# Performance work log

Measured on AMD Instinct MI355X. Metric: run time of the kernel, lower is better.

The kernel has to match this reference:

```python
import jax, jax.numpy as jnp
import numpy as np

B, Tr, P = 256, 512, 128
H, P_STD, P_STATIC, HEAD_H = 128, 32, 16, 64


def _uniform(key, shape, fan_in):
    bound = 1.0 / np.sqrt(fan_in)
    return jax.random.uniform(key, shape, jnp.float32, -bound, bound)


def setup_inputs() -> dict:
    key = jax.random.key(0)
    ks = jax.random.split(key, 16)
    X_raw = jax.random.normal(ks[0], (B, Tr, P), jnp.float32)
    M_raw = (jax.random.uniform(ks[1], (B, Tr, P)) < 0.7).astype(jnp.float32)
    DT_raw = jax.random.uniform(ks[2], (B, Tr, P), jnp.float32)
    STD_agg = jax.random.normal(ks[3], (B, 64, P_STD), jnp.float32)
    Z = jax.random.normal(ks[4], (B, P_STATIC), jnp.float32)
    idx_map = jax.random.randint(ks[5], (B, 64), -1, Tr)  # -1 marks invalid slots
    x_mean = jnp.zeros((P,), jnp.float32)  # non-trainable buffer-like param
    Wd = _uniform(ks[6], (H, P), P)
    bd = _uniform(ks[7], (H,), P)
    Wih = _uniform(ks[8], (3 * H, 2 * P), H)
    bih = _uniform(ks[9], (3 * H,), H)
    Whh = _uniform(ks[10], (3 * H, H), H)
    bhh = _uniform(ks[11], (3 * H,), H)
    W1 = _uniform(ks[12], (HEAD_H, H + P_STD + P_STATIC), H + P_STD + P_STATIC)
    b1 = _uniform(ks[13], (HEAD_H,), H + P_STD + P_STATIC)
    W2 = _uniform(ks[14], (1, HEAD_H), HEAD_H)
    return {"X_raw": X_raw, "M_raw": M_raw, "DT_raw": DT_raw, "STD_agg": STD_agg,
            "Z": Z, "idx_map": idx_map, "x_mean": x_mean, "Wd": Wd, "bd": bd,
            "Wih": Wih, "bih": bih, "Whh": Whh, "bhh": bhh,
            "W1": W1, "b1": b1, "W2": W2}


def reference(X_raw, M_raw, DT_raw, STD_agg, Z, idx_map, x_mean,
              Wd, bd, Wih, bih, Whh, bhh, W1, b1, W2):
    b, tr, p = X_raw.shape
    hdim = Whh.shape[1]

    def step(h, xs):
        x, m, dt = xs  # each [B, p]
        delta = jnp.exp(-jax.nn.softplus(dt))
        x_hat = m * x + (1 - m) * x_mean
        x_dec = m * x + (1 - m) * (delta * x_hat + (1 - delta) * x_mean)
        h_til = jnp.tanh(x_hat @ Wd.T + bd)
        h = delta * h + (1 - delta) * h_til  # requires p == hdim (as in source)
        inp = jnp.concatenate([x_dec, m], axis=-1)  # [B, 2p]
        gi = inp @ Wih.T + bih
        gh = h @ Whh.T + bhh
        gi_r, gi_z, gi_n = jnp.split(gi, 3, axis=-1)
        gh_r, gh_z, gh_n = jnp.split(gh, 3, axis=-1)
        r = jax.nn.sigmoid(gi_r + gh_r)
        z = jax.nn.sigmoid(gi_z + gh_z)
        n = jnp.tanh(gi_n + r * gh_n)
        h = (1 - z) * n + z * h
        return h, h

    h0 = jnp.zeros((b, hdim), X_raw.dtype)
    xs = (jnp.swapaxes(X_raw, 0, 1), jnp.swapaxes(M_raw, 0, 1), jnp.swapaxes(DT_raw, 0, 1))
    _, Hs = jax.lax.scan(step, h0, xs)  # [Tr, B, H]
    H_raw = jnp.swapaxes(Hs, 0, 1)  # [B, Tr, H]

    mask_sel = idx_map >= 0
    idx_safe = jnp.clip(idx_map, 0, None)
    H_agg = jnp.take_along_axis(H_raw, idx_safe[:, :, None], axis=1)
    H_agg = H_agg * mask_sel[:, :, None].astype(H_raw.dtype)  # [B, Ta, H]

    Ta = idx_map.shape[1]
    Zrep = jnp.broadcast_to(Z[:, None, :], (b, Ta, Z.shape[-1]))
    feats = jnp.concatenate([H_agg, STD_agg, Zrep], axis=-1)
    eta = (jax.nn.relu(feats @ W1.T + b1) @ W2.T)[..., 0]  # dropout is identity in eval
    return eta, H_raw, H_agg, mask_sel.astype(X_raw.dtype)
```

## Files before the change

kernel.cpp:

```cpp
#include <hip/hip_runtime.h>
#include <hip/hip_bf16.h>
#include <hip/hip_fp16.h>

#define B_    256
#define TR    512
#define P_    128
#define H_    128
#define NG    384
#define KI    256
#define TA    64
#define PSTD  32
#define PSTAT 16
#define HH    64
#define FDIM  176

#define TB    16
#define NT    (TR/TB)
#define TILE_BYTES 24576

typedef __attribute__((ext_vector_type(8))) short short8;
typedef __attribute__((ext_vector_type(4))) float f32x4;

__device__ __forceinline__ float bf2f(ushort u) {
    union { uint i; float f; } v; v.i = ((uint)u) << 16; return v.f;
}
__device__ __forceinline__ ushort f2bf(float f) {
    union { float f; uint u; } v; v.f = f;
    uint u = v.u;
    uint r = (u + 0x7fffu + ((u >> 16) & 1u)) >> 16;
    return (ushort)r;
}
__device__ __forceinline__ float sigf(float x) {
    return 1.f / (1.f + __expf(-x));
}
__device__ __forceinline__ float tanhf_fast(float x) {
    float ax = fabsf(x);
    float e = __expf(-2.f * ax);
    float r = (1.f - e) / (1.f + e);
    return copysignf(r, x);
}
__device__ __forceinline__ void bar_lds() {
    __asm__ volatile("s_waitcnt lgkmcnt(0)\n\ts_barrier" ::: "memory");
}
__device__ __forceinline__ float dpp_add_xor1(float x) {
    int r = __builtin_amdgcn_mov_dpp(__float_as_int(x), 0xB1, 0xF, 0xF, true);
    return x + __int_as_float(r);
}
__device__ __forceinline__ float dpp_add_xor2(float x) {
    int r = __builtin_amdgcn_mov_dpp(__float_as_int(x), 0x4E, 0xF, 0xF, true);
    return x + __int_as_float(r);
}

__global__ __launch_bounds__(256) void k_convert(
    const float* __restrict__ Wih, const float* __restrict__ Wd,
    ushort* __restrict__ wih_b, ushort* __restrict__ wd_b)
{
    int i = blockIdx.x * 256 + threadIdx.x;
    if (i < NG * KI) wih_b[i] = f2bf(Wih[i]);
    if (i < H_ * P_) wd_b[i]  = f2bf(Wd[i]);
}

#define SA 392

__global__ __launch_bounds__(256, 2) void k_gemm(
    const float* __restrict__ X, const float* __restrict__ M,
    const float* __restrict__ DT, const float* __restrict__ xmean,
    const ushort* __restrict__ wih_b, const ushort* __restrict__ wd_b,
    const float* __restrict__ bih, const float* __restrict__ bd,
    ushort* __restrict__ gi_ws, ushort* __restrict__ htil_ws,
    float* __restrict__ delta_ws)
{
    __shared__ __align__(16) ushort sA[64 * SA];
    const int tid = threadIdx.x;
    const long r0 = (long)blockIdx.x * 64;

    #pragma unroll 4
    for (int i = 0; i < 32; ++i) {
        int idx = i * 256 + tid;
        int rl = idx >> 7, k = idx & 127;
        long g = (r0 + rl) * 128 + k;
        float x = X[g], m = M[g], dt = DT[g], xm = xmean[k];
        float delta = 1.f / (1.f + __expf(dt));
        float xh = m * x + (1.f - m) * xm;
        float xd = m * x + (1.f - m) * (delta * xh + (1.f - delta) * xm);
        sA[rl * SA + k]       = f2bf(xd);
        sA[rl * SA + 128 + k] = f2bf(m);
        sA[rl * SA + 256 + k] = f2bf(xh);
        delta_ws[g] = delta;
    }
    __syncthreads();

    const int wv   = tid >> 6;
    const int lane = tid & 63;
    const int l16  = lane & 15;
    const int q    = lane >> 4;

    f32x4 acc[4][6];
    #pragma unroll
    for (int rt = 0; rt < 4; ++rt)
        #pragma unroll
        for (int nt = 0; nt < 6; ++nt) acc[rt][nt] = (f32x4){0.f, 0.f, 0.f, 0.f};

    const int nb = 96 * wv;
    #pragma unroll
    for (int ks = 0; ks < 8; ++ks) {
        short8 a[4];
        #pragma unroll
        for (int rt = 0; rt < 4; ++rt)
            a[rt] = *(const short8*)&sA[(rt * 16 + l16) * SA + ks * 32 + q * 8];
        #pragma unroll
        for (int nt = 0; nt < 6; ++nt) {
            const short8 b = *(const short8*)&wih_b[(size_t)(nb + nt * 16 + l16) * KI + ks * 32 + q * 8];
            #pragma unroll
            for (int rt = 0; rt < 4; ++rt)
                acc[rt][nt] = __builtin_amdgcn_mfma_f32_16x16x32_bf16(a[rt], b, acc[rt][nt], 0, 0, 0);
        }
    }

    f32x4 acc2[4][2];
    #pragma unroll
    for (int rt = 0; rt < 4; ++rt)
        #pragma unroll
        for (int nt = 0; nt < 2; ++nt) acc2[rt][nt] = (f32x4){0.f, 0.f, 0.f, 0.f};

    const int nb2 = 32 * wv;
    #pragma unroll
    for (int ks = 0; ks < 4; ++ks) {
        short8 a[4];
        #pragma unroll
        for (int rt = 0; rt < 4; ++rt)
            a[rt] = *(const short8*)&sA[(rt * 16 + l16) * SA + 256 + ks * 32 + q * 8];
        #pragma unroll
        for (int nt = 0; nt < 2; ++nt) {
            const short8 b = *(const short8*)&wd_b[(size_t)(nb2 + nt * 16 + l16) * P_ + ks * 32 + q * 8];
            #pragma unroll
            for (int rt = 0; rt < 4; ++rt)
                acc2[rt][nt] = __builtin_amdgcn_mfma_f32_16x16x32_bf16(a[rt], b, acc2[rt][nt], 0, 0, 0);
        }
    }

    __syncthreads();

    ushort* sOut = sA;
    #pragma unroll
    for (int nt = 0; nt < 6; ++nt) {
        const int n = nb + nt * 16 + l16;
        const float bi = bih[n];
        #pragma unroll
        for (int rt = 0; rt < 4; ++rt) {
            #pragma unroll
            for (int reg = 0; reg < 4; ++reg) {
                int row = rt * 16 + q * 4 + reg;
                sOut[row * NG + n] = f2bf(acc[rt][nt][reg] + bi);
            }
        }
    }
    __syncthreads();

    {
        uint4* dst = (uint4*)(gi_ws + (size_t)r0 * NG);
        const uint4* src = (const uint4*)sOut;
        #pragma unroll
        for (int i = 0; i < 12; ++i) dst[tid + 256 * i] = src[tid + 256 * i];
    }
    __syncthreads();

    #pragma unroll
    for (int nt = 0; nt < 2; ++nt) {
        const int n = nb2 + nt * 16 + l16;
        const float bi = bd[n];
        #pragma unroll
        for (int rt = 0; rt < 4; ++rt) {
            #pragma unroll
            for (int reg = 0; reg < 4; ++reg) {
                int row = rt * 16 + q * 4 + reg;
                sOut[row * P_ + n] = f2bf(tanhf_fast(acc2[rt][nt][reg] + bi));
            }
        }
    }
    __syncthreads();

    {
        uint4* dst = (uint4*)(htil_ws + (size_t)r0 * P_);
        const uint4* src = (const uint4*)sOut;
        #pragma unroll
        for (int i = 0; i < 4; ++i) dst[tid + 256 * i] = src[tid + 256 * i];
    }
}

__global__ __launch_bounds__(512, 2) void k_scan(
    const ushort* __restrict__ gi_ws, const ushort* __restrict__ htil_ws,
    const float* __restrict__ delta_ws, const float* __restrict__ Whh,
    const float* __restrict__ bhh, float* __restrict__ Hraw)
{
    __shared__ __align__(16) char  s_in[2][TILE_BYTES];
    __shared__ __align__(16) float s_hout[TB * P_];
    __shared__ __align__(16) float s_hpre[2][144];

    const int tid = threadIdx.x;
    const int b   = blockIdx.x;
    const int j   = tid >> 2;
    const int q   = tid & 3;
    const long base = (long)b * TR;
    const int hpos = 36 * (j >> 5) + (j & 31);

    float4 wv[3][8];
    #pragma unroll
    for (int g = 0; g < 3; ++g) {
        const float4* wp = (const float4*)(Whh + ((g << 7) + j) * H_ + (q << 5));
        #pragma unroll
        for (int i = 0; i < 8; ++i) wv[g][i] = wp[i];
    }
    float bh0 = 0.f, bh1 = 0.f, bh2 = 0.f;
    if (q == 0) { bh0 = bhh[j]; bh1 = bhh[128 + j]; bh2 = bhh[256 + j]; }

    {
        const uint4* gi4 = (const uint4*)(gi_ws   + (size_t)base * NG);
        const uint4* ht4 = (const uint4*)(htil_ws + (size_t)base * P_);
        const uint4* dl4 = (const uint4*)(delta_ws + (size_t)base * P_);
        uint4 p0 = gi4[tid];
        uint4 p1 = (tid < 256) ? gi4[512 + tid] : ht4[tid - 256];
        uint4 p2 = dl4[tid];
        uint4* d = (uint4*)s_in[0];
        d[tid] = p0; d[512 + tid] = p1; d[1024 + tid] = p2;
    }
    bar_lds();

    int cur = 0, sb = 0;
    float h = 0.f, h_pre = 0.f;
    float d_c = 0.f, ht_c = 0.f, gr_c = 0.f, gz_c = 0.f, gn_c = 0.f;

    for (int tile = 0; tile < NT; ++tile) {
        uint4 p0, p1, p2;
        const int has_next = (tile + 1 < NT);
        if (has_next) {
            const long tn = base + (long)(tile + 1) * TB;
            const uint4* gi4 = (const uint4*)(gi_ws   + (size_t)tn * NG);
            const uint4* ht4 = (const uint4*)(htil_ws + (size_t)tn * P_);
            const uint4* dl4 = (const uint4*)(delta_ws + (size_t)tn * P_);
            p0 = gi4[tid];
            p1 = (tid < 256) ? gi4[512 + tid] : ht4[tid - 256];
            p2 = dl4[tid];
        }

        const ushort* sgi = (const ushort*)s_in[cur];
        const ushort* sht = (const ushort*)(s_in[cur] + 12288);
        const float*  sdl = (const float*) (s_in[cur] + 16384);

        if (q == 0) {
            d_c  = sdl[j];
            ht_c = bf2f(sht[j]);
            gr_c = bf2f(sgi[j]);
            gz_c = bf2f(sgi[128 + j]);
            gn_c = bf2f(sgi[256 + j]);
        }

        for (int ts = 0; ts < TB; ++ts) {
            if (q == 0) {
                h_pre = d_c * h + (1.f - d_c) * ht_c;
                s_hpre[sb][hpos] = h_pre;
            }
            bar_lds();

            float d_n = d_c, ht_n = ht_c, gr_n = gr_c, gz_n = gz_c, gn_n = gn_c;
            if (q == 0 && ts + 1 < TB) {
                d_n  = sdl[(ts + 1) * P_ + j];
                ht_n = bf2f(sht[(ts + 1) * P_ + j]);
                gr_n = bf2f(sgi[(ts + 1) * NG + j]);
                gz_n = bf2f(sgi[(ts + 1) * NG + 128 + j]);
                gn_n = bf2f(sgi[(ts + 1) * NG + 256 + j]);
            }

            const float4* hp = (const float4*)&s_hpre[sb][q * 36];
            float ar0 = 0.f, ar1 = 0.f, az0 = 0.f, az1 = 0.f, an0 = 0.f, an1 = 0.f;
            #pragma unroll
            for (int i = 0; i < 8; ++i) {
                float4 hv = hp[i];
                float4 w0 = wv[0][i], w1 = wv[1][i], w2 = wv[2][i];
                float pr = w0.x * hv.x + w0.y * hv.y + w0.z * hv.z + w0.w * hv.w;
                float pz = w1.x * hv.x + w1.y * hv.y + w1.z * hv.z + w1.w * hv.w;
                float pn = w2.x * hv.x + w2.y * hv.y + w2.z * hv.z + w2.w * hv.w;
                if (i & 1) { ar1 += pr; az1 += pz; an1 += pn; }
                else       { ar0 += pr; az0 += pz; an0 += pn; }
            }
            float sr = ar0 + ar1, sz = az0 + az1, sn = an0 + an1;
            sr = dpp_add_xor2(dpp_add_xor1(sr));
            sz = dpp_add_xor2(dpp_add_xor1(sz));
            sn = dpp_add_xor2(dpp_add_xor1(sn));

            if (q == 0) {
                float r = sigf(gr_c + bh0 + sr);
                float z = sigf(gz_c + bh1 + sz);
                float n = tanhf_fast(gn_c + r * (bh2 + sn));
                h = (1.f - z) * n + z * h_pre;
                s_hout[ts * P_ + j] = h;
                d_c = d_n; ht_c = ht_n; gr_c = gr_n; gz_c = gz_n; gn_c = gn_n;
            }
            sb ^= 1;
        }

        bar_lds();

        {
            uint4* dst = (uint4*)(Hraw + (base + (long)tile * TB) * H_);
            dst[tid] = ((const uint4*)s_hout)[tid];
        }
        if (has_next) {
            uint4* d = (uint4*)s_in[cur ^ 1];
            d[tid] = p0; d[512 + tid] = p1; d[1024 + tid] = p2;
        }
        bar_lds();
        cur ^= 1;
    }
}

__global__ __launch_bounds__(256) void k_head(
    const float* __restrict__ Hraw, const float* __restrict__ STD,
    const float* __restrict__ Z, const int* __restrict__ idx_map,
    const float* __restrict__ W1, const float* __restrict__ b1,
    const float* __restrict__ W2,
    float* __restrict__ eta, float* __restrict__ Hagg,
    float* __restrict__ mask_out)
{
    __shared__ float sW1[HH * FDIM];
    __shared__ float sb1[HH], sW2[HH];
    __shared__ float spart[TA][4];

    const int tid = threadIdx.x, b = blockIdx.x;
    for (int i = tid; i < HH * FDIM; i += 256) sW1[i] = W1[i];
    if (tid < HH) { sb1[tid] = b1[tid]; sW2[tid] = W2[tid]; }
    __syncthreads();

    const int s = tid >> 2, p = tid & 3;
    const int idx = idx_map[b * TA + s];
    const int valid = idx >= 0;
    const int tt = valid ? idx : 0;
    const float* hrow = Hraw + ((long)b * TR + tt) * H_;

    float acc[16];
    #pragma unroll
    for (int uu = 0; uu < 16; ++uu) acc[uu] = sb1[p * 16 + uu];

    for (int f = 0; f < FDIM; ++f) {
        float feat;
        if (f < H_)              feat = valid ? hrow[f] : 0.f;
        else if (f < H_ + PSTD)  feat = STD[((long)b * TA + s) * PSTD + (f - H_)];
        else                     feat = Z[b * PSTAT + (f - H_ - PSTD)];
        #pragma unroll
        for (int uu = 0; uu < 16; ++uu)
            acc[uu] += feat * sW1[(p * 16 + uu) * FDIM + f];
    }

    float pe = 0.f;
    #pragma unroll
    for (int uu = 0; uu < 16; ++uu) {
        float a = acc[uu];
        pe += (a > 0.f ? a : 0.f) * sW2[p * 16 + uu];
    }
    spart[s][p] = pe;

    for (int e = 0; e < 32; ++e) {
        int ee = p * 32 + e;
        Hagg[((long)b * TA + s) * H_ + ee] = valid ? hrow[ee] : 0.f;
    }
    if (p == 0) mask_out[b * TA + s] = valid ? 1.f : 0.f;

    __syncthreads();
    if (tid < TA)
        eta[b * TA + tid] = spart[tid][0] + spart[tid][1] + spart[tid][2] + spart[tid][3];
}

extern "C" void kernel_launch(void* const* d_in, const int* in_sizes, int n_in,
                              void* d_out, int out_size, void* d_ws, size_t ws_size,
                              hipStream_t stream)
{
    const float* X     = (const float*)d_in[0];
    const float* M     = (const float*)d_in[1];
    const float* DT    = (const float*)d_in[2];
    const float* STD   = (const float*)d_in[3];
    const float* Z     = (const float*)d_in[4];
    const int*   idxm  = (const int*)  d_in[5];
    const float* xmean = (const float*)d_in[6];
    const float* Wd    = (const float*)d_in[7];
    const float* bd    = (const float*)d_in[8];
    const float* Wih   = (const float*)d_in[9];
    const float* bih   = (const float*)d_in[10];
    const float* Whh   = (const float*)d_in[11];
    const float* bhh   = (const float*)d_in[12];
    const float* W1    = (const float*)d_in[13];
    const float* b1    = (const float*)d_in[14];
    const float* W2    = (const float*)d_in[15];

    const long RROWS = (long)B_ * TR;
    char* ws = (char*)d_ws;
    size_t off = 0;
    ushort* gi_ws   = (ushort*)(ws + off); off += (size_t)RROWS * NG * 2;
    ushort* htil_ws = (ushort*)(ws + off); off += (size_t)RROWS * P_ * 2;
    float*  delta_ws= (float*) (ws + off); off += (size_t)RROWS * P_ * 4;
    ushort* wih_b   = (ushort*)(ws + off); off += (size_t)NG * KI * 2;
    ushort* wd_b    = (ushort*)(ws + off); off += (size_t)H_ * P_ * 2;

    float* out   = (float*)d_out;
    float* eta   = out;
    float* Hraw  = out + 16384;
    float* Hagg  = out + 16384 + (long)B_ * TR * H_;
    float* maskO = Hagg + (long)B_ * TA * H_;

    hipLaunchKernelGGL(k_convert, dim3(384), dim3(256), 0, stream,
                       Wih, Wd, wih_b, wd_b);
    hipLaunchKernelGGL(k_gemm, dim3(2048), dim3(256), 0, stream,
                       X, M, DT, xmean, wih_b, wd_b, bih, bd,
                       gi_ws, htil_ws, delta_ws);
    hipLaunchKernelGGL(k_scan, dim3(256), dim3(512), 0, stream,
                       gi_ws, htil_ws, delta_ws, Whh, bhh, Hraw);
    hipLaunchKernelGGL(k_head, dim3(256), dim3(256), 0, stream,
                       Hraw, STD, Z, idxm, W1, b1, W2, eta, Hagg, maskO);
}
```

Baseline: 774.5 us.

## Rewrite GRU scan as batched MFMA recurrence over eight sequences per block

The recurrent scan now handles 8 batch sequences per 256-thread block. The h·Whh^T product runs on fp16 MFMA, with the weights held in registers as fp16 fragments and the hidden state exchanged through LDS each step. The bhh r/z biases are folded into bih during conversion, so they ride in the gi precomputation. Per-step inputs are prefetched directly from global memory two steps ahead instead of being staged through LDS tiles. This trades the per-thread FMA dot products and DPP reductions for matrix-core throughput, but launches only 32 blocks, wastes half of each 16-wide MFMA tile on padding, and lowers the precision of h to fp16.

```diff
diff --git a/kernel.cpp b/kernel.cpp
--- a/kernel.cpp
+++ b/kernel.cpp
@@ -14,12 +14,13 @@
 #define HH    64
 #define FDIM  176
 
-#define TB    16
-#define NT    (TR/TB)
-#define TILE_BYTES 24576
+#define NB    8
+#define NSCAN (B_/NB)
 
 typedef __attribute__((ext_vector_type(8))) short short8;
 typedef __attribute__((ext_vector_type(4))) float f32x4;
+typedef _Float16 f16;
+typedef __attribute__((ext_vector_type(8))) _Float16 f16x8;
 
 __device__ __forceinline__ float bf2f(ushort u) {
     union { uint i; float f; } v; v.i = ((uint)u) << 16; return v.f;
@@ -30,8 +31,11 @@
     uint r = (u + 0x7fffu + ((u >> 16) & 1u)) >> 16;
     return (ushort)r;
 }
-__device__ __forceinline__ float sigf(float x) {
-    return 1.f / (1.f + __expf(-x));
+__device__ __forceinline__ float bflo(uint u) {
+    union { uint i; float f; } v; v.i = u << 16; return v.f;
+}
+__device__ __forceinline__ float bfhi(uint u) {
+    union { uint i; float f; } v; v.i = u & 0xffff0000u; return v.f;
 }
 __device__ __forceinline__ float tanhf_fast(float x) {
     float ax = fabsf(x);
@@ -39,25 +43,26 @@
     float r = (1.f - e) / (1.f + e);
     return copysignf(r, x);
 }
+__device__ __forceinline__ float sigf2(float x) {
+    return __builtin_amdgcn_rcpf(1.f + __expf(-x));
+}
+__device__ __forceinline__ float tanh2(float x) {
+    return 1.f - 2.f * __builtin_amdgcn_rcpf(1.f + __expf(2.f * x));
+}
 __device__ __forceinline__ void bar_lds() {
     __asm__ volatile("s_waitcnt lgkmcnt(0)\n\ts_barrier" ::: "memory");
 }
-__device__ __forceinline__ float dpp_add_xor1(float x) {
-    int r = __builtin_amdgcn_mov_dpp(__float_as_int(x), 0xB1, 0xF, 0xF, true);
-    return x + __int_as_float(r);
-}
-__device__ __forceinline__ float dpp_add_xor2(float x) {
-    int r = __builtin_amdgcn_mov_dpp(__float_as_int(x), 0x4E, 0xF, 0xF, true);
-    return x + __int_as_float(r);
-}
 
 __global__ __launch_bounds__(256) void k_convert(
     const float* __restrict__ Wih, const float* __restrict__ Wd,
-    ushort* __restrict__ wih_b, ushort* __restrict__ wd_b)
+    const float* __restrict__ bih, const float* __restrict__ bhh,
+    ushort* __restrict__ wih_b, ushort* __restrict__ wd_b,
+    float* __restrict__ bihc)
 {
     int i = blockIdx.x * 256 + threadIdx.x;
     if (i < NG * KI) wih_b[i] = f2bf(Wih[i]);
     if (i < H_ * P_) wd_b[i]  = f2bf(Wd[i]);
+    if (i < NG) bihc[i] = bih[i] + (i < 2 * H_ ? bhh[i] : 0.f);
 }
 
 #define SA 392
@@ -188,129 +193,155 @@
     }
 }
 
-__global__ __launch_bounds__(512, 2) void k_scan(
+
+#define LOADG(PFX, T) if (act) {                                            \
+    const ushort* gp = gptr + (size_t)(T) * NG;                             \
+    const ushort* hp = hptr + (size_t)(T) * P_;                             \
+    const float*  dp = dptr + (size_t)(T) * P_;                             \
+    PFX##_r0 = *(const uint2*)(gp + j0);                                    \
+    PFX##_r1 = *(const uint2*)(gp + j0 + 16);                               \
+    PFX##_z0 = *(const uint2*)(gp + 128 + j0);                              \
+    PFX##_z1 = *(const uint2*)(gp + 128 + j0 + 16);                         \
+    PFX##_n0 = *(const uint2*)(gp + 256 + j0);                              \
+    PFX##_n1 = *(const uint2*)(gp + 256 + j0 + 16);                         \
+    PFX##_h0 = *(const uint2*)(hp + j0);                                    \
+    PFX##_h1 = *(const uint2*)(hp + j0 + 16);                               \
+    PFX##_d0 = *(const float4*)(dp + j0);                                   \
+    PFX##_d1 = *(const float4*)(dp + j0 + 16);                              \
+}
+
+#define STEP(T, BC, BN, PC, PN) {                                           \
+    bar_lds();                                                              \
+    f16x8 bf[4];                                                            \
+    _Pragma("unroll")                                                       \
+    for (int ks = 0; ks < 4; ++ks)                                          \
+        bf[ks] = *(const f16x8*)&h_lds[PC][bb][ks * 32 + q * 8];            \
+    f32x4 ac[3][2];                                                         \
+    ac[0][0] = (f32x4){bflo(BC##_r0.x), bfhi(BC##_r0.x), bflo(BC##_r0.y), bfhi(BC##_r0.y)}; \
+    ac[0][1] = (f32x4){bflo(BC##_r1.x), bfhi(BC##_r1.x), bflo(BC##_r1.y), bfhi(BC##_r1.y)}; \
+    ac[1][0] = (f32x4){bflo(BC##_z0.x), bfhi(BC##_z0.x), bflo(BC##_z0.y), bfhi(BC##_z0.y)}; \
+    ac[1][1] = (f32x4){bflo(BC##_z1.x), bfhi(BC##_z1.x), bflo(BC##_z1.y), bfhi(BC##_z1.y)}; \
+    ac[2][0] = (f32x4){bhn[0][0], bhn[0][1], bhn[0][2], bhn[0][3]};         \
+    ac[2][1] = (f32x4){bhn[1][0], bhn[1][1], bhn[1][2], bhn[1][3]};         \
+    _Pragma("unroll")                                                       \
+    for (int ks = 0; ks < 4; ++ks) {                                        \
+        _Pragma("unroll")                                                   \
+        for (int g = 0; g < 3; ++g) {                                       \
+            ac[g][0] = __builtin_amdgcn_mfma_f32_16x16x32_f16(aF[g][0][ks], bf[ks], ac[g][0], 0, 0, 0); \
+            ac[g][1] = __builtin_amdgcn_mfma_f32_16x16x32_f16(aF[g][1][ks], bf[ks], ac[g][1], 0, 0, 0); \
+        }                                                                   \
+    }                                                                       \
+    if (act) {                                                              \
+        _Pragma("unroll")                                                   \
+        for (int jt = 0; jt < 2; ++jt) {                                    \
+            uint2 gnv = jt ? BC##_n1 : BC##_n0;                             \
+            uint2 htv = jt ? BN##_h1 : BN##_h0;                             \
+            float4 dlv = jt ? BN##_d1 : BN##_d0;                            \
+            float gn_[4] = {bflo(gnv.x), bfhi(gnv.x), bflo(gnv.y), bfhi(gnv.y)}; \
+            float ht_[4] = {bflo(htv.x), bfhi(htv.x), bflo(htv.y), bfhi(htv.y)}; \
+            float dl_[4] = {dlv.x, dlv.y, dlv.z, dlv.w};                    \
+            float hnv[4];                                                   \
+            _Pragma("unroll")                                               \
+            for (int r = 0; r < 4; ++r) {                                   \
+                float rg = sigf2(ac[0][jt][r]);                             \
+                float zg = sigf2(ac[1][jt][r]);                             \
+                float np = gn_[r] + rg * ac[2][jt][r];                      \
+                float ng = tanh2(np);                                       \
+                float hn = ng + zg * (hpre[jt][r] - ng);                    \
+                hnv[r] = hn;                                                \
+                hpre[jt][r] = ht_[r] + dl_[r] * (hn - ht_[r]);              \
+            }                                                               \
+            *(float4*)&Hraw[(rowb + (T)) * P_ + j0 + jt * 16] =             \
+                make_float4(hnv[0], hnv[1], hnv[2], hnv[3]);                \
+            f16 p0 = (f16)hpre[jt][0], p1 = (f16)hpre[jt][1],               \
+                p2 = (f16)hpre[jt][2], p3 = (f16)hpre[jt][3];               \
+            union { f16 h[4]; uint2 u; } pk = {{p0, p1, p2, p3}};           \
+            *(uint2*)&h_lds[PN][bb][j0 + jt * 16] = pk.u;                   \
+        }                                                                   \
+    }                                                                       \
+    if ((T) + 2 < TR) LOADG(BC, (T) + 2);                                   \
+}
+
+__global__ __launch_bounds__(256, 1) void k_scan(
     const ushort* __restrict__ gi_ws, const ushort* __restrict__ htil_ws,
     const float* __restrict__ delta_ws, const float* __restrict__ Whh,
     const float* __restrict__ bhh, float* __restrict__ Hraw)
 {
-    __shared__ __align__(16) char  s_in[2][TILE_BYTES];
-    __shared__ __align__(16) float s_hout[TB * P_];
-    __shared__ __align__(16) float s_hpre[2][144];
-
-    const int tid = threadIdx.x;
-    const int b   = blockIdx.x;
-    const int j   = tid >> 2;
-    const int q   = tid & 3;
-    const long base = (long)b * TR;
-    const int hpos = 36 * (j >> 5) + (j & 31);
-
-    float4 wv[3][8];
-    #pragma unroll
-    for (int g = 0; g < 3; ++g) {
-        const float4* wp = (const float4*)(Whh + ((g << 7) + j) * H_ + (q << 5));
-        #pragma unroll
-        for (int i = 0; i < 8; ++i) wv[g][i] = wp[i];
-    }
-    float bh0 = 0.f, bh1 = 0.f, bh2 = 0.f;
-    if (q == 0) { bh0 = bhh[j]; bh1 = bhh[128 + j]; bh2 = bhh[256 + j]; }
-
-    {
-        const uint4* gi4 = (const uint4*)(gi_ws   + (size_t)base * NG);
-        const uint4* ht4 = (const uint4*)(htil_ws + (size_t)base * P_);
-        const uint4* dl4 = (const uint4*)(delta_ws + (size_t)base * P_);
-        uint4 p0 = gi4[tid];
-        uint4 p1 = (tid < 256) ? gi4[512 + tid] : ht4[tid - 256];
-        uint4 p2 = dl4[tid];
-        uint4* d = (uint4*)s_in[0];
-        d[tid] = p0; d[512 + tid] = p1; d[1024 + tid] = p2;
-    }
-    bar_lds();
-
-    int cur = 0, sb = 0;
-    float h = 0.f, h_pre = 0.f;
-    float d_c = 0.f, ht_c = 0.f, gr_c = 0.f, gz_c = 0.f, gn_c = 0.f;
-
-    for (int tile = 0; tile < NT; ++tile) {
-        uint4 p0, p1, p2;
-        const int has_next = (tile + 1 < NT);
-        if (has_next) {
-            const long tn = base + (long)(tile + 1) * TB;
-            const uint4* gi4 = (const uint4*)(gi_ws   + (size_t)tn * NG);
-            const uint4* ht4 = (const uint4*)(htil_ws + (size_t)tn * P_);
-            const uint4* dl4 = (const uint4*)(delta_ws + (size_t)tn * P_);
-            p0 = gi4[tid];
-            p1 = (tid < 256) ? gi4[512 + tid] : ht4[tid - 256];
-            p2 = dl4[tid];
-        }
-
-        const ushort* sgi = (const ushort*)s_in[cur];
-        const ushort* sht = (const ushort*)(s_in[cur] + 12288);
-        const float*  sdl = (const float*) (s_in[cur] + 16384);
-
-        if (q == 0) {
-            d_c  = sdl[j];
-            ht_c = bf2f(sht[j]);
-            gr_c = bf2f(sgi[j]);
-            gz_c = bf2f(sgi[128 + j]);
-            gn_c = bf2f(sgi[256 + j]);
-        }
-
-        for (int ts = 0; ts < TB; ++ts) {
-            if (q == 0) {
-                h_pre = d_c * h + (1.f - d_c) * ht_c;
-                s_hpre[sb][hpos] = h_pre;
+    __shared__ __align__(16) f16 h_lds[2][16][136];
+
+    const int tid  = threadIdx.x;
+    const int w    = tid >> 6;
+    const int lane = tid & 63;
+    const int bb   = lane & 15;
+    const int q    = lane >> 4;
+    const bool act = bb < NB;
+    const int bbw  = bb & (NB - 1);
+    const int b0   = blockIdx.x * NB;
+    const int j0   = w * 32 + q * 4;
+
+    for (int i = tid; i < 2 * 16 * 136; i += 256) ((f16*)h_lds)[i] = (f16)0.f;
+
+    f16x8 aF[3][2][4];
+    #pragma unroll
+    for (int g = 0; g < 3; ++g)
+        #pragma unroll
+        for (int jt = 0; jt < 2; ++jt) {
+            const float* wr = Whh + (size_t)(g * 128 + w * 32 + jt * 16 + bb) * 128;
+            #pragma unroll
+            for (int ks = 0; ks < 4; ++ks) {
+                float4 a = *(const float4*)(wr + ks * 32 + q * 8);
+                float4 c = *(const float4*)(wr + ks * 32 + q * 8 + 4);
+                f16x8 v;
+                v[0] = (f16)a.x; v[1] = (f16)a.y; v[2] = (f16)a.z; v[3] = (f16)a.w;
+                v[4] = (f16)c.x; v[5] = (f16)c.y; v[6] = (f16)c.z; v[7] = (f16)c.w;
+                aF[g][jt][ks] = v;
             }
-            bar_lds();
-
-            float d_n = d_c, ht_n = ht_c, gr_n = gr_c, gz_n = gz_c, gn_n = gn_c;
-            if (q == 0 && ts + 1 < TB) {
-                d_n  = sdl[(ts + 1) * P_ + j];
-                ht_n = bf2f(sht[(ts + 1) * P_ + j]);
-                gr_n = bf2f(sgi[(ts + 1) * NG + j]);
-                gz_n = bf2f(sgi[(ts + 1) * NG + 128 + j]);
-                gn_n = bf2f(sgi[(ts + 1) * NG + 256 + j]);
-            }
-
-            const float4* hp = (const float4*)&s_hpre[sb][q * 36];
-            float ar0 = 0.f, ar1 = 0.f, az0 = 0.f, az1 = 0.f, an0 = 0.f, an1 = 0.f;
-            #pragma unroll
-            for (int i = 0; i < 8; ++i) {
-                float4 hv = hp[i];
-                float4 w0 = wv[0][i], w1 = wv[1][i], w2 = wv[2][i];
-                float pr = w0.x * hv.x + w0.y * hv.y + w0.z * hv.z + w0.w * hv.w;
-                float pz = w1.x * hv.x + w1.y * hv.y + w1.z * hv.z + w1.w * hv.w;
-                float pn = w2.x * hv.x + w2.y * hv.y + w2.z * hv.z + w2.w * hv.w;
-                if (i & 1) { ar1 += pr; az1 += pz; an1 += pn; }
-                else       { ar0 += pr; az0 += pz; an0 += pn; }
-            }
-            float sr = ar0 + ar1, sz = az0 + az1, sn = an0 + an1;
-            sr = dpp_add_xor2(dpp_add_xor1(sr));
-            sz = dpp_add_xor2(dpp_add_xor1(sz));
-            sn = dpp_add_xor2(dpp_add_xor1(sn));
-
-            if (q == 0) {
-                float r = sigf(gr_c + bh0 + sr);
-                float z = sigf(gz_c + bh1 + sz);
-                float n = tanhf_fast(gn_c + r * (bh2 + sn));
-                h = (1.f - z) * n + z * h_pre;
-                s_hout[ts * P_ + j] = h;
-                d_c = d_n; ht_c = ht_n; gr_c = gr_n; gz_c = gz_n; gn_c = gn_n;
-            }
-            sb ^= 1;
-        }
-
-        bar_lds();
-
-        {
-            uint4* dst = (uint4*)(Hraw + (base + (long)tile * TB) * H_);
-            dst[tid] = ((const uint4*)s_hout)[tid];
-        }
-        if (has_next) {
-            uint4* d = (uint4*)s_in[cur ^ 1];
-            d[tid] = p0; d[512 + tid] = p1; d[1024 + tid] = p2;
-        }
-        bar_lds();
-        cur ^= 1;
+        }
+
+    float bhn[2][4];
+    #pragma unroll
+    for (int jt = 0; jt < 2; ++jt)
+        #pragma unroll
+        for (int r = 0; r < 4; ++r)
+            bhn[jt][r] = bhh[256 + j0 + jt * 16 + r];
+
+    const long rowb = (long)(b0 + bbw) * TR;
+    const ushort* gptr = gi_ws   + rowb * NG;
+    const ushort* hptr = htil_ws + rowb * P_;
+    const float*  dptr = delta_ws + rowb * P_;
+
+    uint2 gA_r0, gA_r1, gA_z0, gA_z1, gA_n0, gA_n1, gA_h0, gA_h1;
+    float4 gA_d0, gA_d1;
+    uint2 gB_r0, gB_r1, gB_z0, gB_z1, gB_n0, gB_n1, gB_h0, gB_h1;
+    float4 gB_d0, gB_d1;
+
+    LOADG(gA, 0);
+    LOADG(gB, 1);
+
+    float hpre[2][4] = {{0.f, 0.f, 0.f, 0.f}, {0.f, 0.f, 0.f, 0.f}};
+
+    __syncthreads();
+
+    if (act) {
+        #pragma unroll
+        for (int jt = 0; jt < 2; ++jt) {
+            uint2 htv = jt ? gA_h1 : gA_h0;
+            float4 dlv = jt ? gA_d1 : gA_d0;
+            float ht_[4] = {bflo(htv.x), bfhi(htv.x), bflo(htv.y), bfhi(htv.y)};
+            float dl_[4] = {dlv.x, dlv.y, dlv.z, dlv.w};
+            #pragma unroll
+            for (int r = 0; r < 4; ++r)
+                hpre[jt][r] = ht_[r] - dl_[r] * ht_[r];
+            f16 p0 = (f16)hpre[jt][0], p1 = (f16)hpre[jt][1],
+                p2 = (f16)hpre[jt][2], p3 = (f16)hpre[jt][3];
+            union { f16 h[4]; uint2 u; } pk = {{p0, p1, p2, p3}};
+            *(uint2*)&h_lds[0][bb][j0 + jt * 16] = pk.u;
+        }
+    }
+
+    for (int t = 0; t < TR; t += 2) {
+        STEP(t,     gA, gB, 0, 1);
+        STEP(t + 1, gB, gA, 1, 0);
     }
 }
 
@@ -399,6 +430,7 @@
     float*  delta_ws= (float*) (ws + off); off += (size_t)RROWS * P_ * 4;
     ushort* wih_b   = (ushort*)(ws + off); off += (size_t)NG * KI * 2;
     ushort* wd_b    = (ushort*)(ws + off); off += (size_t)H_ * P_ * 2;
+    float*  bihc    = (float*) (ws + off); off += (size_t)NG * 4;
 
     float* out   = (float*)d_out;
     float* eta   = out;
@@ -407,11 +439,11 @@
     float* maskO = Hagg + (long)B_ * TA * H_;
 
     hipLaunchKernelGGL(k_convert, dim3(384), dim3(256), 0, stream,
-                       Wih, Wd, wih_b, wd_b);
+                       Wih, Wd, bih, bhh, wih_b, wd_b, bihc);
     hipLaunchKernelGGL(k_gemm, dim3(2048), dim3(256), 0, stream,
-                       X, M, DT, xmean, wih_b, wd_b, bih, bd,
+                       X, M, DT, xmean, wih_b, wd_b, bihc, bd,
                        gi_ws, htil_ws, delta_ws);
-    hipLaunchKernelGGL(k_scan, dim3(256), dim3(512), 0, stream,
+    hipLaunchKernelGGL(k_scan, dim3(NSCAN), dim3(256), 0, stream,
                        gi_ws, htil_ws, delta_ws, Whh, bhh, Hraw);
     hipLaunchKernelGGL(k_head, dim3(256), dim3(256), 0, stream,
                        Hraw, STD, Z, idxm, W1, b1, W2, eta, Hagg, maskO);
```

New measurement: 1.044 ms. 1.35x slower.
